# Kernel tuning notes

Hardware: AMD Instinct MI355X
Metric: run time of the kernel (lower is better)

The kernel has to match this reference:

```python
import jax, jax.numpy as jnp
import numpy as np

T = 6   # n_tokens_per_window
H = 4   # num_heads


def setup_inputs() -> dict:
    key = jax.random.key(0)
    ks = jax.random.split(key, 13)
    B, N, E = 64, 512, 256
    s = 0.05  # small init scale for weight matrices (stability)
    return {
        "x": jax.random.normal(ks[0], (B, N * T, E), jnp.float32),
        "mask": jax.random.randint(ks[1], (B, N * T), 0, 2, jnp.int32),
        "query": jax.random.normal(ks[2], (E,), jnp.float32),  # classification_query (1,1,E) squeezed
        "in_proj_w": jax.random.normal(ks[3], (3 * E, E), jnp.float32) * s,
        "in_proj_b": jnp.zeros((3 * E,), jnp.float32),
        "out_w": jax.random.normal(ks[4], (E, E), jnp.float32) * s,
        "out_b": jnp.zeros((E,), jnp.float32),
        "ln_g": jnp.ones((E,), jnp.float32),
        "ln_b": jnp.zeros((E,), jnp.float32),
        "w1": jax.random.normal(ks[5], (E // 2, E), jnp.float32) * s,
        "b1": jnp.zeros((E // 2,), jnp.float32),
        "w2": jax.random.normal(ks[6], (1, E // 2), jnp.float32) * s,
        "b2": jnp.zeros((1,), jnp.float32),
    }


def reference(x, mask, query, in_proj_w, in_proj_b, out_w, out_b,
              ln_g, ln_b, w1, b1, w2, b2):
    B, S, E = x.shape
    N = S // T
    BN = B * N
    hd = E // H

    xr = x.reshape(BN, T, E)                      # (BN, T, E)
    mr = mask.reshape(BN, T).astype(bool)         # token validity per window
    valid = mr.any(axis=1)                        # (BN,) window validity

    # --- single-query multi-head attention (torch MHA, eval mode) ---
    Wq, Wk, Wv = in_proj_w[:E], in_proj_w[E:2 * E], in_proj_w[2 * E:]
    bq, bk, bv = in_proj_b[:E], in_proj_b[E:2 * E], in_proj_b[2 * E:]
    q = (query @ Wq.T + bq).reshape(H, hd)        # shared learnable query
    k = (xr @ Wk.T + bk).reshape(BN, T, H, hd)
    v = (xr @ Wv.T + bv).reshape(BN, T, H, hd)

    scores = jnp.einsum('hd,bthd->bht', q, k) / np.float32(np.sqrt(hd))
    scores = jnp.where(mr[:, None, :], scores, jnp.float32(-1e9))  # key_padding_mask
    attw = jax.nn.softmax(scores, axis=-1)        # (BN, H, T)
    attn = jnp.einsum('bht,bthd->bhd', attw, v).reshape(BN, E)
    attn = attn @ out_w.T + out_b                 # out_proj

    # --- classifier: LayerNorm -> Linear -> GELU -> Linear ---
    mu = attn.mean(-1, keepdims=True)
    var = ((attn - mu) ** 2).mean(-1, keepdims=True)
    h = (attn - mu) / jnp.sqrt(var + 1e-5) * ln_g + ln_b
    h = jax.nn.gelu(h @ w1.T + b1, approximate=False)
    logits = h @ w2.T + b2                        # (BN, 1)

    # zero-fill fully masked windows (torch: logits[~valid_windows_mask] = 0)
    logits = jnp.where(valid[:, None], logits, jnp.float32(0.0))
    return logits.reshape(B, N)                   # n_classes == 1 -> squeeze
```

## Files before the change

### kernel.cpp

```cpp
#include <hip/hip_runtime.h>
#include <math.h>

#define TT 6
#define HH 4
#define EE 256
#define RB 32
#define PR 16
#define NTHREADS 256

typedef __attribute__((ext_vector_type(8))) short bf16x8;
typedef __attribute__((ext_vector_type(4))) float f32x4;

__device__ __forceinline__ unsigned short f2b(float f) {
    union { float f; unsigned u; } v; v.f = f;
    unsigned u = v.u + 0x7fffu + ((v.u >> 16) & 1u);
    return (unsigned short)(u >> 16);
}
__device__ __forceinline__ float b2f(unsigned short s) {
    union { unsigned u; float f; } v; v.u = ((unsigned)s) << 16;
    return v.f;
}

#define SWT_OFF 0
#define SB_OFF  8192
#define WVB_OFF 8208
#define OWB_OFF 139280
#define W1B_OFF 270352

__global__ void setup_kernel(const float* __restrict__ query,
                             const float* __restrict__ in_proj_w,
                             const float* __restrict__ in_proj_b,
                             const float* __restrict__ out_w,
                             const float* __restrict__ w1,
                             unsigned char* __restrict__ ws)
{
    unsigned short* swt = (unsigned short*)(ws + SWT_OFF);
    float*          sb  = (float*)(ws + SB_OFF);
    unsigned short* wvb = (unsigned short*)(ws + WVB_OFF);
    unsigned short* owb = (unsigned short*)(ws + OWB_OFF);
    unsigned short* w1b = (unsigned short*)(ws + W1B_OFF);

    const int tid = threadIdx.x;
    const int gidx = blockIdx.x * NTHREADS + tid;
    const int gstride = gridDim.x * NTHREADS;

    for (int i = gidx; i < 65536; i += gstride) wvb[i] = f2b(in_proj_w[512 * 256 + i]);
    for (int i = gidx; i < 65536; i += gstride) owb[i] = f2b(out_w[i]);
    for (int i = gidx; i < 32768; i += gstride) w1b[i] = f2b(w1[i]);

    if (blockIdx.x == 0) {
        __shared__ float q[EE];
        float acc = in_proj_b[tid];
        const float* row = in_proj_w + (size_t)tid * EE;
        for (int e = 0; e < EE; ++e) acc += query[e] * row[e];
        q[tid] = acc;
        __syncthreads();
        for (int i = 0; i < 16; ++i) {
            int flat = tid + NTHREADS * i;
            int n = flat >> 8, k = flat & 255;
            float a = 0.f;
            if (n < HH) {
                for (int d = 0; d < 64; ++d)
                    a += q[n * 64 + d] * in_proj_w[(size_t)(EE + n * 64 + d) * EE + k];
            }
            swt[n * EE + k] = f2b(a);
        }
        if (tid < HH) {
            float a = 0.f;
            for (int d = 0; d < 64; ++d) a += q[tid * 64 + d] * in_proj_b[EE + tid * 64 + d];
            sb[tid] = a;
        }
    }
}

#define XS_OFF   0
#define XBT_OFF  49920
#define SCF_OFF  115712
#define AW_OFF   117632
#define VAL_OFF  119168
#define MB_OFF   119296
#define POOL_SZ  119680
#define YB_OFF   0
#define OUTV_OFF 16640
#define LNB_OFF  0
#define HB_OFF   16640

__global__ __launch_bounds__(NTHREADS, 1)
void fused_head_kernel(const float* __restrict__ x,
                       const int* __restrict__ mask,
                       const float* __restrict__ in_proj_b,
                       const float* __restrict__ out_b,
                       const float* __restrict__ ln_g,
                       const float* __restrict__ ln_b,
                       const float* __restrict__ b1,
                       const float* __restrict__ w2,
                       const float* __restrict__ b2,
                       const unsigned char* __restrict__ ws,
                       float* __restrict__ out)
{
    __shared__ __align__(16) unsigned char pool[POOL_SZ];
    unsigned short* xs   = (unsigned short*)(pool + XS_OFF);
    unsigned short* xbt  = (unsigned short*)(pool + XBT_OFF);
    float*          scf  = (float*)(pool + SCF_OFF);
    float*          aw4  = (float*)(pool + AW_OFF);
    float*          vldf = (float*)(pool + VAL_OFF);
    int*            mbuf = (int*)(pool + MB_OFF);
    unsigned short* yb   = (unsigned short*)(pool + YB_OFF);
    float*          outv = (float*)(pool + OUTV_OFF);
    unsigned short* lnb  = (unsigned short*)(pool + LNB_OFF);
    unsigned short* hb   = (unsigned short*)(pool + HB_OFF);

    const unsigned short* swt = (const unsigned short*)(ws + SWT_OFF);
    const float*          sb  = (const float*)(ws + SB_OFF);
    const unsigned short* wvb = (const unsigned short*)(ws + WVB_OFF);
    const unsigned short* owb = (const unsigned short*)(ws + OWB_OFF);
    const unsigned short* w1b = (const unsigned short*)(ws + W1B_OFF);

    const int tid = threadIdx.x;
    const int wv  = tid >> 6;
    const int ln  = tid & 63;
    const int qd  = ln >> 4;
    const int nl  = ln & 15;
    const int chunk0 = blockIdx.x * RB;

    for (int p = 0; p < 2; ++p) {
        const int c0 = chunk0 + p * PR;
        __syncthreads();
        if (tid < PR * TT) mbuf[tid] = mask[(size_t)c0 * TT + tid];
        const float* xp = x + (size_t)c0 * (TT * EE);
        for (int i = 0; i < 24; ++i) {
            int f = i * 1024 + tid * 4;
            float4 v = *(const float4*)(xp + f);
            int r = f >> 8, e = f & 255;
            union { unsigned short u[4]; uint2 v2; } t2;
            t2.u[0] = f2b(v.x); t2.u[1] = f2b(v.y);
            t2.u[2] = f2b(v.z); t2.u[3] = f2b(v.w);
            *(uint2*)(xs + r * 260 + e) = t2.v2;
        }
        __syncthreads();
        for (int mt = wv; mt < 6; mt += 4) {
            f32x4 acc = {0.f, 0.f, 0.f, 0.f};
            for (int kb = 0; kb < EE; kb += 32) {
                bf16x8 a = *(const bf16x8*)(xs + (mt * 16 + nl) * 260 + kb + qd * 8);
                bf16x8 b = *(const bf16x8*)(swt + nl * EE + kb + qd * 8);
                acc = __builtin_amdgcn_mfma_f32_16x16x32_bf16(a, b, acc, 0, 0, 0);
            }
            if (nl < HH) {
#pragma unroll
                for (int i = 0; i < 4; ++i)
                    scf[(mt * 16 + qd * 4 + i) * 5 + nl] = acc[i];
            }
        }
        __syncthreads();
        if (tid < 64) {
            int g = tid >> 2, h = tid & 3;
            const int* mrow = mbuf + g * TT;
            float sbh = sb[h];
            float vs[TT]; float m = -1e30f;
#pragma unroll
            for (int t = 0; t < TT; ++t) {
                float s = scf[(g * TT + t) * 5 + h] * 0.125f + sbh;
                s = mrow[t] ? s : -1e9f;
                vs[t] = s; m = fmaxf(m, s);
            }
            float sum = 0.f;
#pragma unroll
            for (int t = 0; t < TT; ++t) { float e = __expf(vs[t] - m); vs[t] = e; sum += e; }
            float inv = 1.f / sum;
#pragma unroll
            for (int t = 0; t < TT; ++t) aw4[(g * TT + t) * 4 + h] = vs[t] * inv;
            if (h == 0) {
                int vvv = 0;
#pragma unroll
                for (int t = 0; t < TT; ++t) vvv |= mrow[t];
                vldf[p * PR + g] = vvv ? 1.f : 0.f;
            }
        }
        __syncthreads();
        {
            const int e  = (tid & 127) * 2;
            const int g0 = (tid >> 7) * 8;
            for (int gi = 0; gi < 8; ++gi) {
                int g = g0 + gi;
                float a0[HH] = {0.f, 0.f, 0.f, 0.f};
                float a1[HH] = {0.f, 0.f, 0.f, 0.f};
#pragma unroll
                for (int t = 0; t < TT; ++t) {
                    unsigned xp2 = *(const unsigned*)(xs + (g * TT + t) * 260 + e);
                    float x0 = b2f((unsigned short)(xp2 & 0xffffu));
                    float x1 = b2f((unsigned short)(xp2 >> 16));
                    float4 a = *(const float4*)(aw4 + (g * TT + t) * 4);
                    a0[0] += a.x * x0; a0[1] += a.y * x0; a0[2] += a.z * x0; a0[3] += a.w * x0;
                    a1[0] += a.x * x1; a1[1] += a.y * x1; a1[2] += a.z * x1; a1[3] += a.w * x1;
                }
                int grow = p * PR + g;
#pragma unroll
                for (int h = 0; h < HH; ++h) {
                    unsigned pk = (unsigned)f2b(a0[h]) | ((unsigned)f2b(a1[h]) << 16);
                    *(unsigned*)(xbt + grow * 1028 + h * EE + e) = pk;
                }
            }
        }
    }
    __syncthreads();

    {
        const int h = wv;
        f32x4 acc[2][4];
#pragma unroll
        for (int mt = 0; mt < 2; ++mt)
#pragma unroll
            for (int nt = 0; nt < 4; ++nt) acc[mt][nt] = (f32x4){0.f, 0.f, 0.f, 0.f};
        for (int kb = 0; kb < EE; kb += 32) {
            bf16x8 a0 = *(const bf16x8*)(xbt + (nl)      * 1028 + h * EE + kb + qd * 8);
            bf16x8 a1 = *(const bf16x8*)(xbt + (16 + nl) * 1028 + h * EE + kb + qd * 8);
#pragma unroll
            for (int nt = 0; nt < 4; ++nt) {
                int j = h * 64 + nt * 16 + nl;
                bf16x8 b = *(const bf16x8*)(wvb + (size_t)j * EE + kb + qd * 8);
                acc[0][nt] = __builtin_amdgcn_mfma_f32_16x16x32_bf16(a0, b, acc[0][nt], 0, 0, 0);
                acc[1][nt] = __builtin_amdgcn_mfma_f32_16x16x32_bf16(a1, b, acc[1][nt], 0, 0, 0);
            }
        }
#pragma unroll
        for (int mt = 0; mt < 2; ++mt)
#pragma unroll
            for (int nt = 0; nt < 4; ++nt) {
                int j = h * 64 + nt * 16 + nl;
                float bvj = in_proj_b[2 * EE + j];
#pragma unroll
                for (int i = 0; i < 4; ++i)
                    yb[(mt * 16 + qd * 4 + i) * 260 + j] = f2b(acc[mt][nt][i] + bvj);
            }
    }
    __syncthreads();

    {
        f32x4 acc[2][4];
#pragma unroll
        for (int mt = 0; mt < 2; ++mt)
#pragma unroll
            for (int nt = 0; nt < 4; ++nt) acc[mt][nt] = (f32x4){0.f, 0.f, 0.f, 0.f};
        for (int kb = 0; kb < EE; kb += 32) {
            bf16x8 a0 = *(const bf16x8*)(yb + (nl)      * 260 + kb + qd * 8);
            bf16x8 a1 = *(const bf16x8*)(yb + (16 + nl) * 260 + kb + qd * 8);
#pragma unroll
            for (int nt = 0; nt < 4; ++nt) {
                int j = wv * 64 + nt * 16 + nl;
                bf16x8 b = *(const bf16x8*)(owb + (size_t)j * EE + kb + qd * 8);
                acc[0][nt] = __builtin_amdgcn_mfma_f32_16x16x32_bf16(a0, b, acc[0][nt], 0, 0, 0);
                acc[1][nt] = __builtin_amdgcn_mfma_f32_16x16x32_bf16(a1, b, acc[1][nt], 0, 0, 0);
            }
        }
        __syncthreads();
#pragma unroll
        for (int mt = 0; mt < 2; ++mt)
#pragma unroll
            for (int nt = 0; nt < 4; ++nt) {
                int j = wv * 64 + nt * 16 + nl;
                float obj = out_b[j];
#pragma unroll
                for (int i = 0; i < 4; ++i)
                    outv[(mt * 16 + qd * 4 + i) * 260 + j] = acc[mt][nt][i] + obj;
            }
    }
    __syncthreads();

    {
        int g = tid >> 3, kc = tid & 7;
        float vals[32];
        float s = 0.f, ss = 0.f;
#pragma unroll
        for (int i = 0; i < 8; ++i) {
            float4 v = *(const float4*)(outv + g * 260 + kc * 32 + i * 4);
            vals[i * 4 + 0] = v.x; vals[i * 4 + 1] = v.y;
            vals[i * 4 + 2] = v.z; vals[i * 4 + 3] = v.w;
            s += v.x + v.y + v.z + v.w;
            ss += v.x * v.x + v.y * v.y + v.z * v.z + v.w * v.w;
        }
#pragma unroll
        for (int d = 4; d; d >>= 1) { s += __shfl_xor(s, d, 64); ss += __shfl_xor(ss, d, 64); }
        float mu = s * (1.f / EE);
        float var = ss * (1.f / EE) - mu * mu;
        float rstd = rsqrtf(var + 1e-5f);
#pragma unroll
        for (int i = 0; i < 32; i += 2) {
            int j = kc * 32 + i;
            float2 gg = *(const float2*)(ln_g + j);
            float2 bb = *(const float2*)(ln_b + j);
            float o0 = (vals[i]     - mu) * rstd * gg.x + bb.x;
            float o1 = (vals[i + 1] - mu) * rstd * gg.y + bb.y;
            unsigned pk = (unsigned)f2b(o0) | ((unsigned)f2b(o1) << 16);
            *(unsigned*)(lnb + g * 260 + j) = pk;
        }
    }
    __syncthreads();

    {
        f32x4 acc[2][2];
#pragma unroll
        for (int mt = 0; mt < 2; ++mt)
#pragma unroll
            for (int nt = 0; nt < 2; ++nt) acc[mt][nt] = (f32x4){0.f, 0.f, 0.f, 0.f};
        for (int kb = 0; kb < EE; kb += 32) {
            bf16x8 a0 = *(const bf16x8*)(lnb + (nl)      * 260 + kb + qd * 8);
            bf16x8 a1 = *(const bf16x8*)(lnb + (16 + nl) * 260 + kb + qd * 8);
#pragma unroll
            for (int nt = 0; nt < 2; ++nt) {
                int j = wv * 32 + nt * 16 + nl;
                bf16x8 b = *(const bf16x8*)(w1b + (size_t)j * EE + kb + qd * 8);
                acc[0][nt] = __builtin_amdgcn_mfma_f32_16x16x32_bf16(a0, b, acc[0][nt], 0, 0, 0);
                acc[1][nt] = __builtin_amdgcn_mfma_f32_16x16x32_bf16(a1, b, acc[1][nt], 0, 0, 0);
            }
        }
        __syncthreads();
#pragma unroll
        for (int mt = 0; mt < 2; ++mt)
#pragma unroll
            for (int nt = 0; nt < 2; ++nt) {
                int j = wv * 32 + nt * 16 + nl;
                float bj = b1[j];
#pragma unroll
                for (int i = 0; i < 4; ++i) {
                    float sv = acc[mt][nt][i] + bj;
                    float ge = 0.5f * sv * (1.0f + erff(sv * 0.70710678118654752f));
                    hb[(mt * 16 + qd * 4 + i) * 136 + j] = f2b(ge);
                }
            }
    }
    __syncthreads();

    {
        int g = tid >> 3, j0 = (tid & 7) * 16;
        float part = 0.f;
#pragma unroll
        for (int i = 0; i < 16; i += 2) {
            unsigned pk = *(const unsigned*)(hb + g * 136 + j0 + i);
            float h0 = b2f((unsigned short)(pk & 0xffffu));
            float h1 = b2f((unsigned short)(pk >> 16));
            float2 ww = *(const float2*)(w2 + j0 + i);
            part += ww.x * h0 + ww.y * h1;
        }
#pragma unroll
        for (int d = 4; d; d >>= 1) part += __shfl_xor(part, d, 64);
        if ((tid & 7) == 0) out[chunk0 + g] = (part + b2[0]) * vldf[g];
    }
}

extern "C" void kernel_launch(void* const* d_in, const int* in_sizes, int n_in,
                              void* d_out, int out_size, void* d_ws, size_t ws_size,
                              hipStream_t stream) {
    const float* x         = (const float*)d_in[0];
    const int*   mask      = (const int*)d_in[1];
    const float* query     = (const float*)d_in[2];
    const float* in_proj_w = (const float*)d_in[3];
    const float* in_proj_b = (const float*)d_in[4];
    const float* out_w     = (const float*)d_in[5];
    const float* out_b     = (const float*)d_in[6];
    const float* ln_g      = (const float*)d_in[7];
    const float* ln_b      = (const float*)d_in[8];
    const float* w1        = (const float*)d_in[9];
    const float* b1        = (const float*)d_in[10];
    const float* w2        = (const float*)d_in[11];
    const float* b2        = (const float*)d_in[12];
    float* out = (float*)d_out;
    unsigned char* ws = (unsigned char*)d_ws;

    const int BN = out_size;

    setup_kernel<<<128, NTHREADS, 0, stream>>>(query, in_proj_w, in_proj_b, out_w, w1, ws);
    fused_head_kernel<<<BN / RB, NTHREADS, 0, stream>>>(
        x, mask, in_proj_b, out_b, ln_g, ln_b, b1, w2, b2, ws, out);
}
```

Baseline: 396.7 us.

## Halve rows per block for two-block occupancy and parallelize setup folding

Each block of the fused head kernel now handles 16 windows instead of 32. That halves the shared-memory footprint, so launch bounds allow two blocks per CU, and it doubles the grid size, with the MFMA tiles cut to a single M-tile per wave. The setup step is split into a one-block query projection kernel plus a cast kernel that spreads the query-times-key-weight folding across four blocks. This targets the serial single-block setup and low occupancy while streaming x. In exchange, each weight load from L2 is reused across half as many rows, and there is one extra kernel launch.

```diff
diff --git a/kernel.cpp b/kernel.cpp
--- a/kernel.cpp
+++ b/kernel.cpp
@@ -4,8 +4,8 @@
 #define TT 6
 #define HH 4
 #define EE 256
-#define RB 32
-#define PR 16
+#define RB 16
+#define PR 8
 #define NTHREADS 256
 
 typedef __attribute__((ext_vector_type(8))) short bf16x8;
@@ -23,19 +23,44 @@
 
 #define SWT_OFF 0
 #define SB_OFF  8192
-#define WVB_OFF 8208
-#define OWB_OFF 139280
-#define W1B_OFF 270352
-
-__global__ void setup_kernel(const float* __restrict__ query,
-                             const float* __restrict__ in_proj_w,
-                             const float* __restrict__ in_proj_b,
-                             const float* __restrict__ out_w,
-                             const float* __restrict__ w1,
-                             unsigned char* __restrict__ ws)
+#define Q_OFF   8208
+#define WVB_OFF 9232
+#define OWB_OFF 140304
+#define W1B_OFF 271376
+
+__global__ void setup_q(const float* __restrict__ query,
+                        const float* __restrict__ in_proj_w,
+                        const float* __restrict__ in_proj_b,
+                        unsigned char* __restrict__ ws)
+{
+    __shared__ float qs[EE];
+    float* qv = (float*)(ws + Q_OFF);
+    float* sb = (float*)(ws + SB_OFF);
+    const int tid = threadIdx.x;
+    float acc = in_proj_b[tid];
+    const float* row = in_proj_w + (size_t)tid * EE;
+    for (int e = 0; e < EE; e += 4) {
+        float4 w = *(const float4*)(row + e);
+        float4 q = *(const float4*)(query + e);
+        acc += w.x * q.x + w.y * q.y + w.z * q.z + w.w * q.w;
+    }
+    qs[tid] = acc;
+    qv[tid] = acc;
+    __syncthreads();
+    if (tid < HH) {
+        float a = 0.f;
+        for (int d = 0; d < 64; ++d) a += qs[tid * 64 + d] * in_proj_b[EE + tid * 64 + d];
+        sb[tid] = a;
+    }
+}
+
+__global__ void setup_cast(const float* __restrict__ in_proj_w,
+                           const float* __restrict__ out_w,
+                           const float* __restrict__ w1,
+                           unsigned char* __restrict__ ws)
 {
     unsigned short* swt = (unsigned short*)(ws + SWT_OFF);
-    float*          sb  = (float*)(ws + SB_OFF);
+    const float*    qv  = (const float*)(ws + Q_OFF);
     unsigned short* wvb = (unsigned short*)(ws + WVB_OFF);
     unsigned short* owb = (unsigned short*)(ws + OWB_OFF);
     unsigned short* w1b = (unsigned short*)(ws + W1B_OFF);
@@ -48,44 +73,30 @@
     for (int i = gidx; i < 65536; i += gstride) owb[i] = f2b(out_w[i]);
     for (int i = gidx; i < 32768; i += gstride) w1b[i] = f2b(w1[i]);
 
-    if (blockIdx.x == 0) {
-        __shared__ float q[EE];
-        float acc = in_proj_b[tid];
-        const float* row = in_proj_w + (size_t)tid * EE;
-        for (int e = 0; e < EE; ++e) acc += query[e] * row[e];
-        q[tid] = acc;
-        __syncthreads();
-        for (int i = 0; i < 16; ++i) {
-            int flat = tid + NTHREADS * i;
-            int n = flat >> 8, k = flat & 255;
-            float a = 0.f;
-            if (n < HH) {
-                for (int d = 0; d < 64; ++d)
-                    a += q[n * 64 + d] * in_proj_w[(size_t)(EE + n * 64 + d) * EE + k];
-            }
-            swt[n * EE + k] = f2b(a);
-        }
-        if (tid < HH) {
-            float a = 0.f;
-            for (int d = 0; d < 64; ++d) a += q[tid * 64 + d] * in_proj_b[EE + tid * 64 + d];
-            sb[tid] = a;
-        }
+    if (blockIdx.x < HH) {
+        const int n = blockIdx.x;
+        float a = 0.f;
+        for (int d = 0; d < 64; ++d)
+            a += qv[n * 64 + d] * in_proj_w[(size_t)(EE + n * 64 + d) * EE + tid];
+        swt[n * EE + tid] = f2b(a);
+    } else if (blockIdx.x == HH) {
+        for (int i = HH * EE + tid; i < 16 * EE; i += NTHREADS) swt[i] = 0;
     }
 }
 
 #define XS_OFF   0
-#define XBT_OFF  49920
-#define SCF_OFF  115712
-#define AW_OFF   117632
-#define VAL_OFF  119168
-#define MB_OFF   119296
-#define POOL_SZ  119680
+#define XBT_OFF  24960
+#define SCF_OFF  57856
+#define AW_OFF   58816
+#define VAL_OFF  59584
+#define MB_OFF   59648
+#define POOL_SZ  59840
 #define YB_OFF   0
-#define OUTV_OFF 16640
+#define OUTV_OFF 8320
 #define LNB_OFF  0
-#define HB_OFF   16640
-
-__global__ __launch_bounds__(NTHREADS, 1)
+#define HB_OFF   8320
+
+__global__ __launch_bounds__(NTHREADS, 2)
 void fused_head_kernel(const float* __restrict__ x,
                        const int* __restrict__ mask,
                        const float* __restrict__ in_proj_b,
@@ -128,7 +139,7 @@
         __syncthreads();
         if (tid < PR * TT) mbuf[tid] = mask[(size_t)c0 * TT + tid];
         const float* xp = x + (size_t)c0 * (TT * EE);
-        for (int i = 0; i < 24; ++i) {
+        for (int i = 0; i < 12; ++i) {
             int f = i * 1024 + tid * 4;
             float4 v = *(const float4*)(xp + f);
             int r = f >> 8, e = f & 255;
@@ -138,7 +149,8 @@
             *(uint2*)(xs + r * 260 + e) = t2.v2;
         }
         __syncthreads();
-        for (int mt = wv; mt < 6; mt += 4) {
+        if (wv < 3) {
+            const int mt = wv;
             f32x4 acc = {0.f, 0.f, 0.f, 0.f};
             for (int kb = 0; kb < EE; kb += 32) {
                 bf16x8 a = *(const bf16x8*)(xs + (mt * 16 + nl) * 260 + kb + qd * 8);
@@ -152,7 +164,7 @@
             }
         }
         __syncthreads();
-        if (tid < 64) {
+        if (tid < PR * HH) {
             int g = tid >> 2, h = tid & 3;
             const int* mrow = mbuf + g * TT;
             float sbh = sb[h];
@@ -179,8 +191,8 @@
         __syncthreads();
         {
             const int e  = (tid & 127) * 2;
-            const int g0 = (tid >> 7) * 8;
-            for (int gi = 0; gi < 8; ++gi) {
+            const int g0 = (tid >> 7) * 4;
+            for (int gi = 0; gi < 4; ++gi) {
                 int g = g0 + gi;
                 float a0[HH] = {0.f, 0.f, 0.f, 0.f};
                 float a1[HH] = {0.f, 0.f, 0.f, 0.f};
@@ -206,86 +218,73 @@
 
     {
         const int h = wv;
-        f32x4 acc[2][4];
-#pragma unroll
-        for (int mt = 0; mt < 2; ++mt)
-#pragma unroll
-            for (int nt = 0; nt < 4; ++nt) acc[mt][nt] = (f32x4){0.f, 0.f, 0.f, 0.f};
+        f32x4 acc[4];
+#pragma unroll
+        for (int nt = 0; nt < 4; ++nt) acc[nt] = (f32x4){0.f, 0.f, 0.f, 0.f};
         for (int kb = 0; kb < EE; kb += 32) {
-            bf16x8 a0 = *(const bf16x8*)(xbt + (nl)      * 1028 + h * EE + kb + qd * 8);
-            bf16x8 a1 = *(const bf16x8*)(xbt + (16 + nl) * 1028 + h * EE + kb + qd * 8);
+            bf16x8 a = *(const bf16x8*)(xbt + nl * 1028 + h * EE + kb + qd * 8);
 #pragma unroll
             for (int nt = 0; nt < 4; ++nt) {
                 int j = h * 64 + nt * 16 + nl;
                 bf16x8 b = *(const bf16x8*)(wvb + (size_t)j * EE + kb + qd * 8);
-                acc[0][nt] = __builtin_amdgcn_mfma_f32_16x16x32_bf16(a0, b, acc[0][nt], 0, 0, 0);
-                acc[1][nt] = __builtin_amdgcn_mfma_f32_16x16x32_bf16(a1, b, acc[1][nt], 0, 0, 0);
-            }
-        }
-#pragma unroll
-        for (int mt = 0; mt < 2; ++mt)
-#pragma unroll
-            for (int nt = 0; nt < 4; ++nt) {
-                int j = h * 64 + nt * 16 + nl;
-                float bvj = in_proj_b[2 * EE + j];
-#pragma unroll
-                for (int i = 0; i < 4; ++i)
-                    yb[(mt * 16 + qd * 4 + i) * 260 + j] = f2b(acc[mt][nt][i] + bvj);
-            }
-    }
-    __syncthreads();
-
-    {
-        f32x4 acc[2][4];
-#pragma unroll
-        for (int mt = 0; mt < 2; ++mt)
-#pragma unroll
-            for (int nt = 0; nt < 4; ++nt) acc[mt][nt] = (f32x4){0.f, 0.f, 0.f, 0.f};
+                acc[nt] = __builtin_amdgcn_mfma_f32_16x16x32_bf16(a, b, acc[nt], 0, 0, 0);
+            }
+        }
+#pragma unroll
+        for (int nt = 0; nt < 4; ++nt) {
+            int j = h * 64 + nt * 16 + nl;
+            float bvj = in_proj_b[2 * EE + j];
+#pragma unroll
+            for (int i = 0; i < 4; ++i)
+                yb[(qd * 4 + i) * 260 + j] = f2b(acc[nt][i] + bvj);
+        }
+    }
+    __syncthreads();
+
+    {
+        f32x4 acc[4];
+#pragma unroll
+        for (int nt = 0; nt < 4; ++nt) acc[nt] = (f32x4){0.f, 0.f, 0.f, 0.f};
         for (int kb = 0; kb < EE; kb += 32) {
-            bf16x8 a0 = *(const bf16x8*)(yb + (nl)      * 260 + kb + qd * 8);
-            bf16x8 a1 = *(const bf16x8*)(yb + (16 + nl) * 260 + kb + qd * 8);
+            bf16x8 a = *(const bf16x8*)(yb + nl * 260 + kb + qd * 8);
 #pragma unroll
             for (int nt = 0; nt < 4; ++nt) {
                 int j = wv * 64 + nt * 16 + nl;
                 bf16x8 b = *(const bf16x8*)(owb + (size_t)j * EE + kb + qd * 8);
-                acc[0][nt] = __builtin_amdgcn_mfma_f32_16x16x32_bf16(a0, b, acc[0][nt], 0, 0, 0);
-                acc[1][nt] = __builtin_amdgcn_mfma_f32_16x16x32_bf16(a1, b, acc[1][nt], 0, 0, 0);
-            }
-        }
-        __syncthreads();
-#pragma unroll
-        for (int mt = 0; mt < 2; ++mt)
-#pragma unroll
-            for (int nt = 0; nt < 4; ++nt) {
-                int j = wv * 64 + nt * 16 + nl;
-                float obj = out_b[j];
-#pragma unroll
-                for (int i = 0; i < 4; ++i)
-                    outv[(mt * 16 + qd * 4 + i) * 260 + j] = acc[mt][nt][i] + obj;
-            }
-    }
-    __syncthreads();
-
-    {
-        int g = tid >> 3, kc = tid & 7;
-        float vals[32];
+                acc[nt] = __builtin_amdgcn_mfma_f32_16x16x32_bf16(a, b, acc[nt], 0, 0, 0);
+            }
+        }
+#pragma unroll
+        for (int nt = 0; nt < 4; ++nt) {
+            int j = wv * 64 + nt * 16 + nl;
+            float obj = out_b[j];
+#pragma unroll
+            for (int i = 0; i < 4; ++i)
+                outv[(qd * 4 + i) * 260 + j] = acc[nt][i] + obj;
+        }
+    }
+    __syncthreads();
+
+    {
+        int g = tid >> 4, kc = tid & 15;
+        float vals[16];
         float s = 0.f, ss = 0.f;
 #pragma unroll
-        for (int i = 0; i < 8; ++i) {
-            float4 v = *(const float4*)(outv + g * 260 + kc * 32 + i * 4);
+        for (int i = 0; i < 4; ++i) {
+            float4 v = *(const float4*)(outv + g * 260 + kc * 16 + i * 4);
             vals[i * 4 + 0] = v.x; vals[i * 4 + 1] = v.y;
             vals[i * 4 + 2] = v.z; vals[i * 4 + 3] = v.w;
             s += v.x + v.y + v.z + v.w;
             ss += v.x * v.x + v.y * v.y + v.z * v.z + v.w * v.w;
         }
 #pragma unroll
-        for (int d = 4; d; d >>= 1) { s += __shfl_xor(s, d, 64); ss += __shfl_xor(ss, d, 64); }
+        for (int d = 8; d; d >>= 1) { s += __shfl_xor(s, d, 64); ss += __shfl_xor(ss, d, 64); }
         float mu = s * (1.f / EE);
         float var = ss * (1.f / EE) - mu * mu;
         float rstd = rsqrtf(var + 1e-5f);
 #pragma unroll
-        for (int i = 0; i < 32; i += 2) {
-            int j = kc * 32 + i;
+        for (int i = 0; i < 16; i += 2) {
+            int j = kc * 16 + i;
             float2 gg = *(const float2*)(ln_g + j);
             float2 bb = *(const float2*)(ln_b + j);
             float o0 = (vals[i]     - mu) * rstd * gg.x + bb.x;
@@ -297,44 +296,37 @@
     __syncthreads();
 
     {
-        f32x4 acc[2][2];
-#pragma unroll
-        for (int mt = 0; mt < 2; ++mt)
-#pragma unroll
-            for (int nt = 0; nt < 2; ++nt) acc[mt][nt] = (f32x4){0.f, 0.f, 0.f, 0.f};
+        f32x4 acc[2];
+#pragma unroll
+        for (int nt = 0; nt < 2; ++nt) acc[nt] = (f32x4){0.f, 0.f, 0.f, 0.f};
         for (int kb = 0; kb < EE; kb += 32) {
-            bf16x8 a0 = *(const bf16x8*)(lnb + (nl)      * 260 + kb + qd * 8);
-            bf16x8 a1 = *(const bf16x8*)(lnb + (16 + nl) * 260 + kb + qd * 8);
+            bf16x8 a = *(const bf16x8*)(lnb + nl * 260 + kb + qd * 8);
 #pragma unroll
             for (int nt = 0; nt < 2; ++nt) {
                 int j = wv * 32 + nt * 16 + nl;
                 bf16x8 b = *(const bf16x8*)(w1b + (size_t)j * EE + kb + qd * 8);
-                acc[0][nt] = __builtin_amdgcn_mfma_f32_16x16x32_bf16(a0, b, acc[0][nt], 0, 0, 0);
-                acc[1][nt] = __builtin_amdgcn_mfma_f32_16x16x32_bf16(a1, b, acc[1][nt], 0, 0, 0);
-            }
-        }
-        __syncthreads();
-#pragma unroll
-        for (int mt = 0; mt < 2; ++mt)
-#pragma unroll
-            for (int nt = 0; nt < 2; ++nt) {
-                int j = wv * 32 + nt * 16 + nl;
-                float bj = b1[j];
-#pragma unroll
-                for (int i = 0; i < 4; ++i) {
-                    float sv = acc[mt][nt][i] + bj;
-                    float ge = 0.5f * sv * (1.0f + erff(sv * 0.70710678118654752f));
-                    hb[(mt * 16 + qd * 4 + i) * 136 + j] = f2b(ge);
-                }
-            }
-    }
-    __syncthreads();
-
-    {
-        int g = tid >> 3, j0 = (tid & 7) * 16;
+                acc[nt] = __builtin_amdgcn_mfma_f32_16x16x32_bf16(a, b, acc[nt], 0, 0, 0);
+            }
+        }
+#pragma unroll
+        for (int nt = 0; nt < 2; ++nt) {
+            int j = wv * 32 + nt * 16 + nl;
+            float bj = b1[j];
+#pragma unroll
+            for (int i = 0; i < 4; ++i) {
+                float sv = acc[nt][i] + bj;
+                float ge = 0.5f * sv * (1.0f + erff(sv * 0.70710678118654752f));
+                hb[(qd * 4 + i) * 136 + j] = f2b(ge);
+            }
+        }
+    }
+    __syncthreads();
+
+    {
+        int g = tid >> 4, j0 = (tid & 15) * 8;
         float part = 0.f;
 #pragma unroll
-        for (int i = 0; i < 16; i += 2) {
+        for (int i = 0; i < 8; i += 2) {
             unsigned pk = *(const unsigned*)(hb + g * 136 + j0 + i);
             float h0 = b2f((unsigned short)(pk & 0xffffu));
             float h1 = b2f((unsigned short)(pk >> 16));
@@ -342,8 +334,8 @@
             part += ww.x * h0 + ww.y * h1;
         }
 #pragma unroll
-        for (int d = 4; d; d >>= 1) part += __shfl_xor(part, d, 64);
-        if ((tid & 7) == 0) out[chunk0 + g] = (part + b2[0]) * vldf[g];
+        for (int d = 8; d; d >>= 1) part += __shfl_xor(part, d, 64);
+        if ((tid & 15) == 0) out[chunk0 + g] = (part + b2[0]) * vldf[g];
     }
 }
 
@@ -368,7 +360,8 @@
 
     const int BN = out_size;
 
-    setup_kernel<<<128, NTHREADS, 0, stream>>>(query, in_proj_w, in_proj_b, out_w, w1, ws);
+    setup_q<<<1, NTHREADS, 0, stream>>>(query, in_proj_w, in_proj_b, ws);
+    setup_cast<<<128, NTHREADS, 0, stream>>>(in_proj_w, out_w, w1, ws);
     fused_head_kernel<<<BN / RB, NTHREADS, 0, stream>>>(
         x, mask, in_proj_b, out_b, ln_g, ln_b, b1, w2, b2, ws, out);
 }
```

Result: no change. 394.8 us (-0.5%).
